# Kernel optimization log

Hardware: AMD Instinct MI355X
Metric: run time of the kernel (lower is better)

Reference implementation:

```python
import jax, jax.numpy as jnp
import numpy as np

N_ORDER = 64
SEQ_LEN = 4096
BATCH = 256


def _hippo_scale_buffers(N: int, L: int):
    """Build bilinear-discretized scaled-Legendre (HiPPO-LegS) transition buffers."""
    q = np.arange(N, dtype=np.float64)
    col, row = np.meshgrid(q, q)  # col[i,j]=j, row[i,j]=i
    r = 2 * q + 1
    M = -(np.where(row >= col, r, 0) - np.diag(q))
    T = np.sqrt(np.diag(2 * q + 1))
    A = T @ M @ np.linalg.inv(T)              # (N,N) continuous-time A
    Bv = np.sqrt(2 * q + 1)                   # diag(T) -> continuous-time B vector
    t = np.arange(1, L + 1, dtype=np.float64)
    A_sc = A[None, :, :] / t[:, None, None]   # (L,N,N)
    B_sc = Bv[None, :] / t[:, None]           # (L,N)
    I = np.eye(N, dtype=np.float64)
    Mm = I[None] - 0.5 * A_sc
    Nn = I[None] + 0.5 * A_sc
    A_d = np.linalg.solve(Mm, Nn)                        # (L,N,N)
    B_d = np.linalg.solve(Mm, B_sc[..., None])[..., 0]   # (L,N)
    return A_d.astype(np.float32), B_d.astype(np.float32)


def setup_inputs() -> dict:
    key = jax.random.key(0)
    inputs = jax.random.normal(key, (SEQ_LEN, BATCH), dtype=jnp.float32)
    A_np, B_np = _hippo_scale_buffers(N_ORDER, SEQ_LEN)
    return {
        "inputs": inputs,
        "A_stacked": jnp.asarray(A_np),   # (L,N,N)
        "B_stacked": jnp.asarray(B_np),   # (L,N)
    }


def reference(inputs, A_stacked, B_stacked):
    """x_t = A_t @ x_{t-1} + B_t * inputs_t, x_{-1} = 0. Returns (L, B, N)."""
    L = inputs.shape[0]
    # u[t, b, :] = inputs[t, b] * B_stacked[t, :]
    u = inputs[..., None] * B_stacked[:L, None, :]  # (L,B,N)

    def step(x, au):
        A_t, u_t = au                                  # (N,N), (B,N)
        x = u_t + jnp.einsum('ij,bj->bi', A_t, x)      # (B,N)
        return x, x

    x0 = jnp.zeros(u.shape[1:], dtype=u.dtype)
    _, xs = jax.lax.scan(step, x0, (A_stacked[:L], u))
    return xs  # (L,B,N)
```

## Files before the change

kernel.cpp:

```cpp
#include <hip/hip_runtime.h>
#include <cstdint>


#define TID ((int)threadIdx.x)

typedef _Float16 half8 __attribute__((ext_vector_type(8)));
typedef _Float16 half4v __attribute__((ext_vector_type(4)));
typedef float f32x4 __attribute__((ext_vector_type(4)));

constexpr int SUBL  = 16;
constexpr int PAD   = 68;

constexpr size_t WS_W = 0;
constexpr size_t WS_Q = 262144;
constexpr size_t WS_P = WS_Q + 1048576;
constexpr size_t WS_Z = WS_P + 262144;
constexpr size_t WS_H = WS_Z + 1048576;
constexpr size_t OLD_WS_FLOATS = WS_H + 1048576;

constexpr int SLOT   = 20480;
constexpr int APITCH = 144;
constexpr int AL_OFF = 9216;
constexpr int BV_OFF = 18432;
constexpr int U_OFF  = 18688;
constexpr size_t AWS_BYTES = (size_t)4096 * SLOT;

__device__ __forceinline__ void stage64x64(const float* __restrict__ g, float* __restrict__ l) {
#pragma unroll
  for (int r = 0; r < 4; ++r) {
    int id = TID + 256 * r;
    int i = id >> 4, j0 = (id & 15) << 2;
    *reinterpret_cast<float4*>(&l[i * PAD + j0]) =
        *reinterpret_cast<const float4*>(&g[i * 64 + j0]);
  }
}

__device__ __forceinline__ void matmul_tile(const float* __restrict__ Ml,
                                            const float* __restrict__ Al,
                                            float* __restrict__ Dl,
                                            int i_lo, int i_hi) {
  float acc[4][4];
#pragma unroll
  for (int a = 0; a < 4; ++a)
#pragma unroll
    for (int b = 0; b < 4; ++b) acc[a][b] = 0.f;
  const int j0 = i_hi << 2;
#pragma unroll
  for (int kq = 0; kq < 16; ++kq) {
    const int k0 = kq << 2;
    float4 mf[4], af[4];
#pragma unroll
    for (int a = 0; a < 4; ++a)
      mf[a] = *reinterpret_cast<const float4*>(&Ml[(i_lo + 16 * a) * PAD + k0]);
#pragma unroll
    for (int kk = 0; kk < 4; ++kk)
      af[kk] = *reinterpret_cast<const float4*>(&Al[(k0 + kk) * PAD + j0]);
#pragma unroll
    for (int a = 0; a < 4; ++a) {
      acc[a][0] += mf[a].x * af[0].x + mf[a].y * af[1].x + mf[a].z * af[2].x + mf[a].w * af[3].x;
      acc[a][1] += mf[a].x * af[0].y + mf[a].y * af[1].y + mf[a].z * af[2].y + mf[a].w * af[3].y;
      acc[a][2] += mf[a].x * af[0].z + mf[a].y * af[1].z + mf[a].z * af[2].z + mf[a].w * af[3].z;
      acc[a][3] += mf[a].x * af[0].w + mf[a].y * af[1].w + mf[a].z * af[2].w + mf[a].w * af[3].w;
    }
  }
#pragma unroll
  for (int a = 0; a < 4; ++a)
    *reinterpret_cast<float4*>(&Dl[(i_lo + 16 * a) * PAD + j0]) =
        make_float4(acc[a][0], acc[a][1], acc[a][2], acc[a][3]);
}

__global__ __launch_bounds__(256) void k0_prep(const float* __restrict__ Ag,
                                               const float* __restrict__ Bg,
                                               const float* __restrict__ inp,
                                               unsigned char* __restrict__ Aws) {
  const int t = blockIdx.x;
  unsigned char* slot = Aws + (size_t)t * SLOT;
  const int i = TID >> 2, jq = TID & 3, j0 = jq << 4;
  const float* arow = Ag + (size_t)t * 4096 + i * 64 + j0;
  half8 hv[2], lv[2];
#pragma unroll
  for (int hf = 0; hf < 2; ++hf) {
#pragma unroll
    for (int r = 0; r < 2; ++r) {
      float4 v = *reinterpret_cast<const float4*>(arow + hf * 8 + r * 4);
      float vv[4] = {v.x, v.y, v.z, v.w};
#pragma unroll
      for (int e = 0; e < 4; ++e) {
        _Float16 h = (_Float16)vv[e];
        hv[hf][r * 4 + e] = h;
        lv[hf][r * 4 + e] = (_Float16)(vv[e] - (float)h);
      }
    }
  }
  *reinterpret_cast<half8*>(slot + i * APITCH + j0 * 2)           = hv[0];
  *reinterpret_cast<half8*>(slot + i * APITCH + j0 * 2 + 16)      = hv[1];
  *reinterpret_cast<half8*>(slot + AL_OFF + i * APITCH + j0 * 2)      = lv[0];
  *reinterpret_cast<half8*>(slot + AL_OFF + i * APITCH + j0 * 2 + 16) = lv[1];
  if (jq == 3) {
    half8 z = {};
    *reinterpret_cast<half8*>(slot + i * APITCH + 128) = z;
    *reinterpret_cast<half8*>(slot + AL_OFF + i * APITCH + 128) = z;
  }
  if (TID < 16)
    *reinterpret_cast<float4*>(slot + BV_OFF + TID * 16) =
        *reinterpret_cast<const float4*>(Bg + (size_t)t * 64 + TID * 4);
  if (TID >= 64 && TID < 128) {
    int q = TID - 64;
    *reinterpret_cast<float4*>(slot + U_OFF + q * 16) =
        *reinterpret_cast<const float4*>(inp + (size_t)t * 256 + q * 4);
  }
}

__global__ __launch_bounds__(256) void k1_suffix(const float* __restrict__ Ag,
                                                 const float* __restrict__ Bg,
                                                 float* __restrict__ W,
                                                 float* __restrict__ Qw) {
  __shared__ float Ms[2][64 * PAD];
  __shared__ float As[64 * PAD];
  __shared__ float Bvs[64];
  const int c = blockIdx.x;
  const int i_lo = TID & 15, i_hi = TID >> 4;
  for (int idx = TID; idx < 64 * PAD; idx += 256) Ms[0][idx] = 0.f;
  __syncthreads();
  if (TID < 64) Ms[0][TID * PAD + TID] = 1.f;
  int cur = 0;
  for (int k = SUBL - 1; k >= 0; --k) {
    const int t = c * SUBL + k;
    stage64x64(Ag + (size_t)t * 4096, As);
    if (TID < 16)
      *reinterpret_cast<float4*>(&Bvs[TID * 4]) =
          *reinterpret_cast<const float4*>(&Bg[t * 64 + TID * 4]);
    __syncthreads();
    if (TID < 64) {
      float wv = 0.f;
#pragma unroll
      for (int kq = 0; kq < 16; ++kq) {
        float4 m = *reinterpret_cast<const float4*>(&Ms[cur][TID * PAD + kq * 4]);
        float4 b = *reinterpret_cast<const float4*>(&Bvs[kq * 4]);
        wv += m.x * b.x + m.y * b.y + m.z * b.z + m.w * b.w;
      }
      W[t * 64 + TID] = wv;
    }
    matmul_tile(Ms[cur], As, Ms[cur ^ 1], i_lo, i_hi);
    __syncthreads();
    cur ^= 1;
  }
#pragma unroll
  for (int r = 0; r < 4; ++r) {
    int id = TID + 256 * r;
    int i = id >> 4, j0 = (id & 15) << 2;
    *reinterpret_cast<float4*>(&Qw[(size_t)c * 4096 + i * 64 + j0]) =
        *reinterpret_cast<const float4*>(&Ms[cur][i * PAD + j0]);
  }
}

__global__ __launch_bounds__(256) void k1b_combine(const float* __restrict__ Qw,
                                                   float* __restrict__ W,
                                                   float* __restrict__ Pw) {
  __shared__ float R[2][64 * PAD];
  __shared__ float Qs[64 * PAD];
  __shared__ float wm[16 * PAD];
  const int s = blockIdx.x;
  const int i_lo = TID & 15, i_hi = TID >> 4;
  int cur = 0;
  for (int m = 3; m >= 0; --m) {
    const int c = 4 * s + m;
    stage64x64(Qw + (size_t)c * 4096, Qs);
    {
      int tt = TID >> 4, i0 = (TID & 15) << 2;
      *reinterpret_cast<float4*>(&wm[tt * PAD + i0]) =
          *reinterpret_cast<const float4*>(&W[(size_t)(c * 16 + tt) * 64 + i0]);
    }
    __syncthreads();
    if (m < 3) {
      float acc[4] = {0.f, 0.f, 0.f, 0.f};
#pragma unroll
      for (int kq = 0; kq < 16; ++kq) {
        const int k0 = kq << 2;
        float4 wf = *reinterpret_cast<const float4*>(&wm[i_hi * PAD + k0]);
#pragma unroll
        for (int a = 0; a < 4; ++a) {
          float4 rf = *reinterpret_cast<const float4*>(&R[cur][(i_lo + 16 * a) * PAD + k0]);
          acc[a] += rf.x * wf.x + rf.y * wf.y + rf.z * wf.z + rf.w * wf.w;
        }
      }
#pragma unroll
      for (int a = 0; a < 4; ++a)
        W[(size_t)(c * 16 + i_hi) * 64 + i_lo + 16 * a] = acc[a];
      matmul_tile(R[cur], Qs, R[cur ^ 1], i_lo, i_hi);
    } else {
#pragma unroll
      for (int r = 0; r < 4; ++r) {
        int id = TID + 256 * r;
        int i = id >> 4, j0 = (id & 15) << 2;
        *reinterpret_cast<float4*>(&R[cur ^ 1][i * PAD + j0]) =
            *reinterpret_cast<const float4*>(&Qs[i * PAD + j0]);
      }
    }
    __syncthreads();
    cur ^= 1;
  }
#pragma unroll
  for (int r = 0; r < 4; ++r) {
    int id = TID + 256 * r;
    int i = id >> 4, j0 = (id & 15) << 2;
    *reinterpret_cast<float4*>(&Pw[(size_t)s * 4096 + i * 64 + j0]) =
        *reinterpret_cast<const float4*>(&R[cur][i * PAD + j0]);
  }
}

__global__ __launch_bounds__(256) void k1c_zgemm(const float* __restrict__ inp,
                                                 const float* __restrict__ W,
                                                 float* __restrict__ Zw) {
  __shared__ float inT[64 * PAD];
  __shared__ float wm[64 * PAD];
  const int s = blockIdx.x >> 2, g = blockIdx.x & 3;
  const int b0 = 64 * g, t0 = s * 64;
  const int i_lo = TID & 15, i_hi = TID >> 4;
#pragma unroll
  for (int r = 0; r < 4; ++r) {
    int id = TID + 256 * r;
    int tl = id >> 4, b4 = (id & 15) << 2;
    float4 v = *reinterpret_cast<const float4*>(&inp[(size_t)(t0 + tl) * 256 + b0 + b4]);
    inT[(b4 + 0) * PAD + tl] = v.x;
    inT[(b4 + 1) * PAD + tl] = v.y;
    inT[(b4 + 2) * PAD + tl] = v.z;
    inT[(b4 + 3) * PAD + tl] = v.w;
  }
#pragma unroll
  for (int r = 0; r < 4; ++r) {
    int id = TID + 256 * r;
    int tl = id >> 4, i0 = (id & 15) << 2;
    *reinterpret_cast<float4*>(&wm[tl * PAD + i0]) =
        *reinterpret_cast<const float4*>(&W[(size_t)(t0 + tl) * 64 + i0]);
  }
  __syncthreads();
  float acc[4][4];
#pragma unroll
  for (int a = 0; a < 4; ++a)
#pragma unroll
    for (int q = 0; q < 4; ++q) acc[a][q] = 0.f;
  const int j0c = i_hi << 2;
#pragma unroll
  for (int kq = 0; kq < 16; ++kq) {
    const int k0 = kq << 2;
    float4 bf[4], wf[4];
#pragma unroll
    for (int a = 0; a < 4; ++a)
      bf[a] = *reinterpret_cast<const float4*>(&inT[(i_lo + 16 * a) * PAD + k0]);
#pragma unroll
    for (int kk = 0; kk < 4; ++kk)
      wf[kk] = *reinterpret_cast<const float4*>(&wm[(k0 + kk) * PAD + j0c]);
#pragma unroll
    for (int a = 0; a < 4; ++a) {
      acc[a][0] += bf[a].x * wf[0].x + bf[a].y * wf[1].x + bf[a].z * wf[2].x + bf[a].w * wf[3].x;
      acc[a][1] += bf[a].x * wf[0].y + bf[a].y * wf[1].y + bf[a].z * wf[2].y + bf[a].w * wf[3].y;
      acc[a][2] += bf[a].x * wf[0].z + bf[a].y * wf[1].z + bf[a].z * wf[2].z + bf[a].w * wf[3].z;
      acc[a][3] += bf[a].x * wf[0].w + bf[a].y * wf[1].w + bf[a].z * wf[2].w + bf[a].w * wf[3].w;
    }
  }
  __syncthreads();
#pragma unroll
  for (int a = 0; a < 4; ++a)
    *reinterpret_cast<float4*>(&wm[(i_lo + 16 * a) * PAD + j0c]) =
        make_float4(acc[a][0], acc[a][1], acc[a][2], acc[a][3]);
  __syncthreads();
#pragma unroll
  for (int r = 0; r < 4; ++r) {
    int id = TID + 256 * r;
    int bl = id >> 4, i0 = (id & 15) << 2;
    *reinterpret_cast<float4*>(&Zw[(size_t)s * 16384 + (b0 + bl) * 64 + i0]) =
        *reinterpret_cast<const float4*>(&wm[bl * PAD + i0]);
  }
}

__global__ __launch_bounds__(256) void k2_carry(const float* __restrict__ Pw,
                                                const float* __restrict__ Zw,
                                                float* __restrict__ Hw) {
  __shared__ float Pt[64 * PAD];
  __shared__ float xb[4 * PAD];
  const int g = blockIdx.x;
  const int bl = TID >> 6, i = TID & 63;
  const int bg = 4 * g + bl;
  for (int idx = TID; idx < 4 * PAD; idx += 256) xb[idx] = 0.f;
#pragma unroll
  for (int r = 0; r < 4; ++r) {
    int id = TID + 256 * r;
    int ir = id >> 4, j0 = (id & 15) << 2;
    float4 v = *reinterpret_cast<const float4*>(&Pw[ir * 64 + j0]);
    Pt[(j0 + 0) * PAD + ir] = v.x;
    Pt[(j0 + 1) * PAD + ir] = v.y;
    Pt[(j0 + 2) * PAD + ir] = v.z;
    Pt[(j0 + 3) * PAD + ir] = v.w;
  }
  __syncthreads();
  float h = 0.f;
  for (int s = 0; s < 64; ++s) {
    Hw[(size_t)s * 16384 + bg * 64 + i] = h;
    float acc = Zw[(size_t)s * 16384 + bg * 64 + i];
#pragma unroll
    for (int jq = 0; jq < 16; ++jq) {
      const int j0 = jq << 2;
      float4 xf = *reinterpret_cast<const float4*>(&xb[bl * PAD + j0]);
      acc += Pt[(j0 + 0) * PAD + i] * xf.x + Pt[(j0 + 1) * PAD + i] * xf.y +
             Pt[(j0 + 2) * PAD + i] * xf.z + Pt[(j0 + 3) * PAD + i] * xf.w;
    }
    h = acc;
    __syncthreads();
    xb[bl * PAD + i] = h;
    if (s < 63) {
#pragma unroll
      for (int r = 0; r < 4; ++r) {
        int id = TID + 256 * r;
        int ir = id >> 4, j0 = (id & 15) << 2;
        float4 v = *reinterpret_cast<const float4*>(&Pw[(size_t)(s + 1) * 4096 + ir * 64 + j0]);
        Pt[(j0 + 0) * PAD + ir] = v.x;
        Pt[(j0 + 1) * PAD + ir] = v.y;
        Pt[(j0 + 2) * PAD + ir] = v.z;
        Pt[(j0 + 3) * PAD + ir] = v.w;
      }
    }
    __syncthreads();
  }
}

__global__ __launch_bounds__(256) void k3_final(const float* __restrict__ Ag,
                                                const float* __restrict__ Bg,
                                                const float* __restrict__ inp,
                                                const float* __restrict__ Hw,
                                                float* __restrict__ out) {
  __shared__ float As[64 * PAD];
  __shared__ float xs[64 * PAD];
  __shared__ float Bvs[64];
  __shared__ float ins[64];
  const int s = blockIdx.x >> 2, g = blockIdx.x & 3;
  const int b0 = 64 * g;
  const int i_lo = TID & 15, i_hi = TID >> 4;
#pragma unroll
  for (int r = 0; r < 4; ++r) {
    int id = TID + 256 * r;
    int bl = id >> 4, i0 = (id & 15) << 2;
    *reinterpret_cast<float4*>(&xs[bl * PAD + i0]) =
        *reinterpret_cast<const float4*>(&Hw[(size_t)s * 16384 + (b0 + bl) * 64 + i0]);
  }
  for (int k = 0; k < 64; ++k) {
    const int t = s * 64 + k;
    stage64x64(Ag + (size_t)t * 4096, As);
    if (TID < 16)
      *reinterpret_cast<float4*>(&Bvs[TID * 4]) =
          *reinterpret_cast<const float4*>(&Bg[t * 64 + TID * 4]);
    if (TID >= 64 && TID < 80) {
      int q = TID - 64;
      *reinterpret_cast<float4*>(&ins[q * 4]) =
          *reinterpret_cast<const float4*>(&inp[(size_t)t * 256 + b0 + q * 4]);
    }
    __syncthreads();
    float acc[4][4];
#pragma unroll
    for (int a = 0; a < 4; ++a)
#pragma unroll
      for (int r = 0; r < 4; ++r) acc[a][r] = 0.f;
#pragma unroll
    for (int jq = 0; jq < 16; ++jq) {
      const int j0 = jq << 2;
      float4 af[4], xf[4];
#pragma unroll
      for (int a = 0; a < 4; ++a)
        af[a] = *reinterpret_cast<const float4*>(&As[(i_lo + 16 * a) * PAD + j0]);
#pragma unroll
      for (int r = 0; r < 4; ++r)
        xf[r] = *reinterpret_cast<const float4*>(&xs[(i_hi + 16 * r) * PAD + j0]);
#pragma unroll
      for (int a = 0; a < 4; ++a)
#pragma unroll
        for (int r = 0; r < 4; ++r)
          acc[a][r] += af[a].x * xf[r].x + af[a].y * xf[r].y + af[a].z * xf[r].z + af[a].w * xf[r].w;
    }
    float bv[4], ui[4];
#pragma unroll
    for (int a = 0; a < 4; ++a) bv[a] = Bvs[i_lo + 16 * a];
#pragma unroll
    for (int r = 0; r < 4; ++r) ui[r] = ins[i_hi + 16 * r];
#pragma unroll
    for (int a = 0; a < 4; ++a)
#pragma unroll
      for (int r = 0; r < 4; ++r) acc[a][r] += bv[a] * ui[r];
    __syncthreads();
#pragma unroll
    for (int r = 0; r < 4; ++r)
#pragma unroll
      for (int a = 0; a < 4; ++a)
        xs[(i_hi + 16 * r) * PAD + i_lo + 16 * a] = acc[a][r];
    __syncthreads();
#pragma unroll
    for (int r = 0; r < 4; ++r) {
      int id = TID + 256 * r;
      int bl = id >> 4, i0 = (id & 15) << 2;
      *reinterpret_cast<float4*>(&out[((size_t)t * 256 + b0 + bl) * 64 + i0]) =
          *reinterpret_cast<const float4*>(&xs[bl * PAD + i0]);
    }
  }
}

__device__ __forceinline__ void gload_lds16(const void* g, void* l) {
  __builtin_amdgcn_global_load_lds(
      (const __attribute__((address_space(1))) unsigned int*)g,
      (__attribute__((address_space(3))) unsigned int*)l, 16, 0, 0);
}

constexpr int LDS_XH = 2 * SLOT;
constexpr int LDS_XL = LDS_XH + 9216;
constexpr int LDS_SZ = LDS_XL + 9216;

__global__ __launch_bounds__(256) void k3_mfma(const unsigned char* __restrict__ Aws,
                                               const float* __restrict__ Hw,
                                               float* __restrict__ out) {
  __shared__ __align__(16) unsigned char sm[LDS_SZ];
  const int blk = blockIdx.x;
  const int s = (blk & 7) | ((blk >> 5) << 3);
  const int g = (blk >> 3) & 3;
  const int b0 = g << 6;
  const int lane = TID & 63, wave = TID >> 6;
  const int lm = lane & 15, quad = lane >> 4;
  const int wm = wave >> 1, wn = wave & 1;

#pragma unroll
  for (int r = 0; r < 4; ++r) {
    int id = TID + (r << 8);
    int bl = id >> 4, j0 = (id & 15) << 2;
    float4 v = *reinterpret_cast<const float4*>(
        &Hw[(size_t)s * 16384 + (size_t)(b0 + bl) * 64 + j0]);
    float vv[4] = {v.x, v.y, v.z, v.w};
    half4v hh, ll;
#pragma unroll
    for (int e = 0; e < 4; ++e) {
      _Float16 h = (_Float16)vv[e];
      hh[e] = h;
      ll[e] = (_Float16)(vv[e] - (float)h);
    }
    *reinterpret_cast<half4v*>(sm + LDS_XH + bl * APITCH + (j0 << 1)) = hh;
    *reinterpret_cast<half4v*>(sm + LDS_XL + bl * APITCH + (j0 << 1)) = ll;
  }

  const size_t t0 = (size_t)s * 64;
  {
    const unsigned char* gsl = Aws + t0 * SLOT;
#pragma unroll
    for (int r = 0; r < 5; ++r) {
      int off = ((r << 2) + wave) << 10;
      gload_lds16(gsl + off + lane * 16, sm + off);
    }
  }

  int aoff[2][2], xoffh[2][2], xoffl[2][2], woff[2][2];
#pragma unroll
  for (int mt = 0; mt < 2; ++mt)
#pragma unroll
    for (int kt = 0; kt < 2; ++kt)
      aoff[mt][kt] = ((wm << 5) + (mt << 4) + lm) * APITCH + (((kt << 5) + (quad << 3)) << 1);
#pragma unroll
  for (int nt = 0; nt < 2; ++nt)
#pragma unroll
    for (int kt = 0; kt < 2; ++kt) {
      int o = ((wn << 5) + (nt << 4) + lm) * APITCH + (((kt << 5) + (quad << 3)) << 1);
      xoffh[nt][kt] = LDS_XH + o;
      xoffl[nt][kt] = LDS_XL + o;
    }
#pragma unroll
  for (int nt = 0; nt < 2; ++nt)
#pragma unroll
    for (int mt = 0; mt < 2; ++mt)
      woff[nt][mt] = ((wn << 5) + (nt << 4) + lm) * APITCH +
                     (((wm << 5) + (mt << 4) + (quad << 2)) << 1);

  __syncthreads();

  int cur = 0;
  for (int k = 0; k < 64; ++k) {
    const unsigned char* ab = sm + cur * SLOT;
    if (k < 63) {
      const unsigned char* gsl = Aws + (t0 + k + 1) * SLOT;
      unsigned char* lb = sm + (cur ^ 1) * SLOT;
#pragma unroll
      for (int r = 0; r < 5; ++r) {
        int off = ((r << 2) + wave) << 10;
        gload_lds16(gsl + off + lane * 16, lb + off);
      }
    }
    half8 fa[2][2], fal[2][2], fxh[2][2], fxl[2][2];
#pragma unroll
    for (int mt = 0; mt < 2; ++mt)
#pragma unroll
      for (int kt = 0; kt < 2; ++kt) {
        fa[mt][kt]  = *reinterpret_cast<const half8*>(ab + aoff[mt][kt]);
        fal[mt][kt] = *reinterpret_cast<const half8*>(ab + AL_OFF + aoff[mt][kt]);
      }
#pragma unroll
    for (int nt = 0; nt < 2; ++nt)
#pragma unroll
      for (int kt = 0; kt < 2; ++kt) {
        fxh[nt][kt] = *reinterpret_cast<const half8*>(sm + xoffh[nt][kt]);
        fxl[nt][kt] = *reinterpret_cast<const half8*>(sm + xoffl[nt][kt]);
      }
    float4 bv[2];
#pragma unroll
    for (int mt = 0; mt < 2; ++mt)
      bv[mt] = *reinterpret_cast<const float4*>(
          ab + BV_OFF + (((wm << 5) + (mt << 4) + (quad << 2)) << 2));
    float uu[2];
#pragma unroll
    for (int nt = 0; nt < 2; ++nt)
      uu[nt] = *reinterpret_cast<const float*>(
          ab + U_OFF + ((b0 + (wn << 5) + (nt << 4) + lm) << 2));

    f32x4 acc[2][2] = {};
#pragma unroll
    for (int mt = 0; mt < 2; ++mt)
#pragma unroll
      for (int nt = 0; nt < 2; ++nt)
#pragma unroll
        for (int kt = 0; kt < 2; ++kt) {
          acc[mt][nt] = __builtin_amdgcn_mfma_f32_16x16x32_f16(fa[mt][kt],  fxh[nt][kt], acc[mt][nt], 0, 0, 0);
          acc[mt][nt] = __builtin_amdgcn_mfma_f32_16x16x32_f16(fal[mt][kt], fxh[nt][kt], acc[mt][nt], 0, 0, 0);
          acc[mt][nt] = __builtin_amdgcn_mfma_f32_16x16x32_f16(fa[mt][kt],  fxl[nt][kt], acc[mt][nt], 0, 0, 0);
        }
#pragma unroll
    for (int mt = 0; mt < 2; ++mt) {
      const float* bp = reinterpret_cast<const float*>(&bv[mt]);
#pragma unroll
      for (int nt = 0; nt < 2; ++nt)
#pragma unroll
        for (int e = 0; e < 4; ++e) acc[mt][nt][e] += bp[e] * uu[nt];
    }
    __syncthreads();
#pragma unroll
    for (int mt = 0; mt < 2; ++mt)
#pragma unroll
      for (int nt = 0; nt < 2; ++nt) {
        half4v hh, ll;
#pragma unroll
        for (int e = 0; e < 4; ++e) {
          float x = acc[mt][nt][e];
          _Float16 h = (_Float16)x;
          hh[e] = h;
          ll[e] = (_Float16)(x - (float)h);
        }
        *reinterpret_cast<half4v*>(sm + LDS_XH + woff[nt][mt]) = hh;
        *reinterpret_cast<half4v*>(sm + LDS_XL + woff[nt][mt]) = ll;
        const int bglob = b0 + (wn << 5) + (nt << 4) + lm;
        const int irow = (wm << 5) + (mt << 4) + (quad << 2);
        *reinterpret_cast<float4*>(&out[(((t0 + k) << 8) + bglob) * 64 + irow]) =
            make_float4(acc[mt][nt][0], acc[mt][nt][1], acc[mt][nt][2], acc[mt][nt][3]);
      }
    __syncthreads();
    cur ^= 1;
  }
}

extern "C" void kernel_launch(void* const* d_in, const int* in_sizes, int n_in,
                              void* d_out, int out_size, void* d_ws, size_t ws_size,
                              hipStream_t stream) {
  const float* inputs = (const float*)d_in[0];
  const float* Ag     = (const float*)d_in[1];
  const float* Bg     = (const float*)d_in[2];
  float* out = (float*)d_out;

  const bool use_mfma = ws_size >= AWS_BYTES + OLD_WS_FLOATS * 4;
  unsigned char* Aws = (unsigned char*)d_ws;
  float* ws = (float*)((char*)d_ws + (use_mfma ? AWS_BYTES : 0));
  float* W  = ws + WS_W;
  float* Qw = ws + WS_Q;
  float* Pw = ws + WS_P;
  float* Zw = ws + WS_Z;
  float* Hw = ws + WS_H;

  if (use_mfma) k0_prep<<<4096, 256, 0, stream>>>(Ag, Bg, inputs, Aws);
  k1_suffix<<<256, 256, 0, stream>>>(Ag, Bg, W, Qw);
  k1b_combine<<<64, 256, 0, stream>>>(Qw, W, Pw);
  k1c_zgemm<<<256, 256, 0, stream>>>(inputs, W, Zw);
  k2_carry<<<64, 256, 0, stream>>>(Pw, Zw, Hw);
  if (use_mfma)
    k3_mfma<<<256, 256, 0, stream>>>(Aws, Hw, out);
  else
    k3_final<<<256, 256, 0, stream>>>(Ag, Bg, inputs, Hw, out);
}
```

Before: 644.8 us.

## Fuse A-prep into suffix kernel, prefetch carry loads, split final MFMA grid

The separate A_t split/conversion kernel is folded into the suffix-product kernel, so each A_t is read from global memory once and written out as hi/lo fp16 in the same pass that forms the chunk products. The suffix kernel also double-buffers A_t and B_t in shared memory, and the carry kernel prefetches the next P and Z values into registers before the current step. The final MFMA kernel halves the batch tile per block to 32 columns and launches 512 blocks with two blocks per CU, trading per-block reuse for more parallelism. This removes one launch and one full read of A, at the cost of more shared memory and register use in the fused kernel.

```diff
diff --git a/kernel.cpp b/kernel.cpp
--- a/kernel.cpp
+++ b/kernel.cpp
@@ -69,45 +69,109 @@
         make_float4(acc[a][0], acc[a][1], acc[a][2], acc[a][3]);
 }
 
-__global__ __launch_bounds__(256) void k0_prep(const float* __restrict__ Ag,
-                                               const float* __restrict__ Bg,
-                                               const float* __restrict__ inp,
-                                               unsigned char* __restrict__ Aws) {
-  const int t = blockIdx.x;
-  unsigned char* slot = Aws + (size_t)t * SLOT;
-  const int i = TID >> 2, jq = TID & 3, j0 = jq << 4;
-  const float* arow = Ag + (size_t)t * 4096 + i * 64 + j0;
-  half8 hv[2], lv[2];
-#pragma unroll
-  for (int hf = 0; hf < 2; ++hf) {
-#pragma unroll
-    for (int r = 0; r < 2; ++r) {
-      float4 v = *reinterpret_cast<const float4*>(arow + hf * 8 + r * 4);
-      float vv[4] = {v.x, v.y, v.z, v.w};
+__global__ __launch_bounds__(256) void k1_fused(const float* __restrict__ Ag,
+                                                const float* __restrict__ Bg,
+                                                const float* __restrict__ inp,
+                                                unsigned char* __restrict__ Aws,
+                                                float* __restrict__ W,
+                                                float* __restrict__ Qw) {
+  __shared__ float Ms[2][64 * PAD];
+  __shared__ float As[2][64 * PAD];
+  __shared__ float Bvs[2][64];
+  const int c = blockIdx.x;
+  const int i_lo = TID & 15, i_hi = TID >> 4;
+  const int r_i0 = TID >> 4;
+  const int r_j0 = (TID & 15) << 2;
+
+  for (int idx = TID; idx < 64 * PAD; idx += 256) Ms[0][idx] = 0.f;
+
+  float4 pc[4];
+  float4 bvc = make_float4(0.f, 0.f, 0.f, 0.f);
+  {
+    const float* g = Ag + (size_t)(c * SUBL + SUBL - 1) * 4096;
+#pragma unroll
+    for (int r = 0; r < 4; ++r)
+      pc[r] = *reinterpret_cast<const float4*>(&g[(r_i0 + 16 * r) * 64 + r_j0]);
+    if (TID < 16)
+      bvc = *reinterpret_cast<const float4*>(&Bg[(size_t)(c * SUBL + SUBL - 1) * 64 + TID * 4]);
+  }
+  __syncthreads();
+  if (TID < 64) Ms[0][TID * PAD + TID] = 1.f;
+#pragma unroll
+  for (int r = 0; r < 4; ++r)
+    *reinterpret_cast<float4*>(&As[0][(r_i0 + 16 * r) * PAD + r_j0]) = pc[r];
+  if (TID < 16) *reinterpret_cast<float4*>(&Bvs[0][TID * 4]) = bvc;
+  __syncthreads();
+
+  int cur = 0, ab = 0;
+  for (int k = SUBL - 1; k >= 0; --k) {
+    const int t = c * SUBL + k;
+    unsigned char* slot = Aws + (size_t)t * SLOT;
+    float4 pn[4];
+    float4 bvn = make_float4(0.f, 0.f, 0.f, 0.f);
+    if (k > 0) {
+      const float* g = Ag + (size_t)(t - 1) * 4096;
+#pragma unroll
+      for (int r = 0; r < 4; ++r)
+        pn[r] = *reinterpret_cast<const float4*>(&g[(r_i0 + 16 * r) * 64 + r_j0]);
+      if (TID < 16)
+        bvn = *reinterpret_cast<const float4*>(&Bg[(size_t)(t - 1) * 64 + TID * 4]);
+    }
+    if (TID >= 64 && TID < 128) {
+      int q = TID - 64;
+      *reinterpret_cast<float4*>(slot + U_OFF + q * 16) =
+          *reinterpret_cast<const float4*>(inp + (size_t)t * 256 + q * 4);
+    }
+    if (TID < 16) *reinterpret_cast<float4*>(slot + BV_OFF + TID * 16) = bvc;
+    if (TID < 64) {
+      float wv = 0.f;
+#pragma unroll
+      for (int kq = 0; kq < 16; ++kq) {
+        float4 m = *reinterpret_cast<const float4*>(&Ms[cur][TID * PAD + kq * 4]);
+        float4 b = *reinterpret_cast<const float4*>(&Bvs[ab][kq * 4]);
+        wv += m.x * b.x + m.y * b.y + m.z * b.z + m.w * b.w;
+      }
+      W[t * 64 + TID] = wv;
+    }
+#pragma unroll
+    for (int r = 0; r < 4; ++r) {
+      float vv[4] = {pc[r].x, pc[r].y, pc[r].z, pc[r].w};
+      half4v hh, ll;
 #pragma unroll
       for (int e = 0; e < 4; ++e) {
         _Float16 h = (_Float16)vv[e];
-        hv[hf][r * 4 + e] = h;
-        lv[hf][r * 4 + e] = (_Float16)(vv[e] - (float)h);
-      }
-    }
-  }
-  *reinterpret_cast<half8*>(slot + i * APITCH + j0 * 2)           = hv[0];
-  *reinterpret_cast<half8*>(slot + i * APITCH + j0 * 2 + 16)      = hv[1];
-  *reinterpret_cast<half8*>(slot + AL_OFF + i * APITCH + j0 * 2)      = lv[0];
-  *reinterpret_cast<half8*>(slot + AL_OFF + i * APITCH + j0 * 2 + 16) = lv[1];
-  if (jq == 3) {
-    half8 z = {};
-    *reinterpret_cast<half8*>(slot + i * APITCH + 128) = z;
-    *reinterpret_cast<half8*>(slot + AL_OFF + i * APITCH + 128) = z;
-  }
-  if (TID < 16)
-    *reinterpret_cast<float4*>(slot + BV_OFF + TID * 16) =
-        *reinterpret_cast<const float4*>(Bg + (size_t)t * 64 + TID * 4);
-  if (TID >= 64 && TID < 128) {
-    int q = TID - 64;
-    *reinterpret_cast<float4*>(slot + U_OFF + q * 16) =
-        *reinterpret_cast<const float4*>(inp + (size_t)t * 256 + q * 4);
+        hh[e] = h;
+        ll[e] = (_Float16)(vv[e] - (float)h);
+      }
+      const int row = r_i0 + 16 * r;
+      *reinterpret_cast<half4v*>(slot + row * APITCH + r_j0 * 2) = hh;
+      *reinterpret_cast<half4v*>(slot + AL_OFF + row * APITCH + r_j0 * 2) = ll;
+    }
+    if (TID < 64) {
+      half8 z = {};
+      *reinterpret_cast<half8*>(slot + TID * APITCH + 128) = z;
+      *reinterpret_cast<half8*>(slot + AL_OFF + TID * APITCH + 128) = z;
+    }
+    matmul_tile(Ms[cur], As[ab], Ms[cur ^ 1], i_lo, i_hi);
+    if (k > 0) {
+#pragma unroll
+      for (int r = 0; r < 4; ++r)
+        *reinterpret_cast<float4*>(&As[ab ^ 1][(r_i0 + 16 * r) * PAD + r_j0]) = pn[r];
+      if (TID < 16) *reinterpret_cast<float4*>(&Bvs[ab ^ 1][TID * 4]) = bvn;
+#pragma unroll
+      for (int r = 0; r < 4; ++r) pc[r] = pn[r];
+      bvc = bvn;
+    }
+    __syncthreads();
+    cur ^= 1;
+    ab ^= 1;
+  }
+#pragma unroll
+  for (int r = 0; r < 4; ++r) {
+    int id = TID + 256 * r;
+    int i = id >> 4, j0 = (id & 15) << 2;
+    *reinterpret_cast<float4*>(&Qw[(size_t)c * 4096 + i * 64 + j0]) =
+        *reinterpret_cast<const float4*>(&Ms[cur][i * PAD + j0]);
   }
 }
 
@@ -282,28 +346,41 @@
   const int g = blockIdx.x;
   const int bl = TID >> 6, i = TID & 63;
   const int bg = 4 * g + bl;
+  const int ir = TID >> 4, j0 = (TID & 15) << 2;
   for (int idx = TID; idx < 4 * PAD; idx += 256) xb[idx] = 0.f;
-#pragma unroll
-  for (int r = 0; r < 4; ++r) {
-    int id = TID + 256 * r;
-    int ir = id >> 4, j0 = (id & 15) << 2;
-    float4 v = *reinterpret_cast<const float4*>(&Pw[ir * 64 + j0]);
-    Pt[(j0 + 0) * PAD + ir] = v.x;
-    Pt[(j0 + 1) * PAD + ir] = v.y;
-    Pt[(j0 + 2) * PAD + ir] = v.z;
-    Pt[(j0 + 3) * PAD + ir] = v.w;
+  float4 p0[4];
+#pragma unroll
+  for (int r = 0; r < 4; ++r)
+    p0[r] = *reinterpret_cast<const float4*>(&Pw[(ir + 16 * r) * 64 + j0]);
+  float zc = Zw[(size_t)bg * 64 + i];
+#pragma unroll
+  for (int r = 0; r < 4; ++r) {
+    int row = ir + 16 * r;
+    Pt[(j0 + 0) * PAD + row] = p0[r].x;
+    Pt[(j0 + 1) * PAD + row] = p0[r].y;
+    Pt[(j0 + 2) * PAD + row] = p0[r].z;
+    Pt[(j0 + 3) * PAD + row] = p0[r].w;
   }
   __syncthreads();
   float h = 0.f;
   for (int s = 0; s < 64; ++s) {
+    float4 pn[4];
+    float zn = 0.f;
+    if (s < 63) {
+#pragma unroll
+      for (int r = 0; r < 4; ++r)
+        pn[r] = *reinterpret_cast<const float4*>(
+            &Pw[(size_t)(s + 1) * 4096 + (ir + 16 * r) * 64 + j0]);
+      zn = Zw[(size_t)(s + 1) * 16384 + bg * 64 + i];
+    }
     Hw[(size_t)s * 16384 + bg * 64 + i] = h;
-    float acc = Zw[(size_t)s * 16384 + bg * 64 + i];
+    float acc = zc;
 #pragma unroll
     for (int jq = 0; jq < 16; ++jq) {
-      const int j0 = jq << 2;
-      float4 xf = *reinterpret_cast<const float4*>(&xb[bl * PAD + j0]);
-      acc += Pt[(j0 + 0) * PAD + i] * xf.x + Pt[(j0 + 1) * PAD + i] * xf.y +
-             Pt[(j0 + 2) * PAD + i] * xf.z + Pt[(j0 + 3) * PAD + i] * xf.w;
+      const int jj = jq << 2;
+      float4 xf = *reinterpret_cast<const float4*>(&xb[bl * PAD + jj]);
+      acc += Pt[(jj + 0) * PAD + i] * xf.x + Pt[(jj + 1) * PAD + i] * xf.y +
+             Pt[(jj + 2) * PAD + i] * xf.z + Pt[(jj + 3) * PAD + i] * xf.w;
     }
     h = acc;
     __syncthreads();
@@ -311,14 +388,13 @@
     if (s < 63) {
 #pragma unroll
       for (int r = 0; r < 4; ++r) {
-        int id = TID + 256 * r;
-        int ir = id >> 4, j0 = (id & 15) << 2;
-        float4 v = *reinterpret_cast<const float4*>(&Pw[(size_t)(s + 1) * 4096 + ir * 64 + j0]);
-        Pt[(j0 + 0) * PAD + ir] = v.x;
-        Pt[(j0 + 1) * PAD + ir] = v.y;
-        Pt[(j0 + 2) * PAD + ir] = v.z;
-        Pt[(j0 + 3) * PAD + ir] = v.w;
-      }
+        int row = ir + 16 * r;
+        Pt[(j0 + 0) * PAD + row] = pn[r].x;
+        Pt[(j0 + 1) * PAD + row] = pn[r].y;
+        Pt[(j0 + 2) * PAD + row] = pn[r].z;
+        Pt[(j0 + 3) * PAD + row] = pn[r].w;
+      }
+      zc = zn;
     }
     __syncthreads();
   }
@@ -408,24 +484,25 @@
       (__attribute__((address_space(3))) unsigned int*)l, 16, 0, 0);
 }
 
+constexpr int XROWS  = 32;
 constexpr int LDS_XH = 2 * SLOT;
-constexpr int LDS_XL = LDS_XH + 9216;
-constexpr int LDS_SZ = LDS_XL + 9216;
-
-__global__ __launch_bounds__(256) void k3_mfma(const unsigned char* __restrict__ Aws,
-                                               const float* __restrict__ Hw,
-                                               float* __restrict__ out) {
+constexpr int LDS_XL = LDS_XH + XROWS * APITCH;
+constexpr int LDS_SZ = LDS_XL + XROWS * APITCH;
+
+__global__ __launch_bounds__(256, 2) void k3_mfma(const unsigned char* __restrict__ Aws,
+                                                  const float* __restrict__ Hw,
+                                                  float* __restrict__ out) {
   __shared__ __align__(16) unsigned char sm[LDS_SZ];
   const int blk = blockIdx.x;
-  const int s = (blk & 7) | ((blk >> 5) << 3);
-  const int g = (blk >> 3) & 3;
-  const int b0 = g << 6;
+  const int s = (blk & 7) | ((blk >> 6) << 3);
+  const int g = (blk >> 3) & 7;
+  const int b0 = g << 5;
   const int lane = TID & 63, wave = TID >> 6;
   const int lm = lane & 15, quad = lane >> 4;
   const int wm = wave >> 1, wn = wave & 1;
 
 #pragma unroll
-  for (int r = 0; r < 4; ++r) {
+  for (int r = 0; r < 2; ++r) {
     int id = TID + (r << 8);
     int bl = id >> 4, j0 = (id & 15) << 2;
     float4 v = *reinterpret_cast<const float4*>(
@@ -452,26 +529,21 @@
     }
   }
 
-  int aoff[2][2], xoffh[2][2], xoffl[2][2], woff[2][2];
+  int aoff[2][2], xoffh[2], xoffl[2], woff[2];
 #pragma unroll
   for (int mt = 0; mt < 2; ++mt)
 #pragma unroll
     for (int kt = 0; kt < 2; ++kt)
       aoff[mt][kt] = ((wm << 5) + (mt << 4) + lm) * APITCH + (((kt << 5) + (quad << 3)) << 1);
 #pragma unroll
-  for (int nt = 0; nt < 2; ++nt)
-#pragma unroll
-    for (int kt = 0; kt < 2; ++kt) {
-      int o = ((wn << 5) + (nt << 4) + lm) * APITCH + (((kt << 5) + (quad << 3)) << 1);
-      xoffh[nt][kt] = LDS_XH + o;
-      xoffl[nt][kt] = LDS_XL + o;
-    }
-#pragma unroll
-  for (int nt = 0; nt < 2; ++nt)
-#pragma unroll
-    for (int mt = 0; mt < 2; ++mt)
-      woff[nt][mt] = ((wn << 5) + (nt << 4) + lm) * APITCH +
-                     (((wm << 5) + (mt << 4) + (quad << 2)) << 1);
+  for (int kt = 0; kt < 2; ++kt) {
+    int o = ((wn << 4) + lm) * APITCH + (((kt << 5) + (quad << 3)) << 1);
+    xoffh[kt] = LDS_XH + o;
+    xoffl[kt] = LDS_XL + o;
+  }
+#pragma unroll
+  for (int mt = 0; mt < 2; ++mt)
+    woff[mt] = ((wn << 4) + lm) * APITCH + (((wm << 5) + (mt << 4) + (quad << 2)) << 1);
 
   __syncthreads();
 
@@ -487,7 +559,7 @@
         gload_lds16(gsl + off + lane * 16, lb + off);
       }
     }
-    half8 fa[2][2], fal[2][2], fxh[2][2], fxl[2][2];
+    half8 fa[2][2], fal[2][2], fxh[2], fxl[2];
 #pragma unroll
     for (int mt = 0; mt < 2; ++mt)
 #pragma unroll
@@ -496,62 +568,51 @@
         fal[mt][kt] = *reinterpret_cast<const half8*>(ab + AL_OFF + aoff[mt][kt]);
       }
 #pragma unroll
-    for (int nt = 0; nt < 2; ++nt)
-#pragma unroll
-      for (int kt = 0; kt < 2; ++kt) {
-        fxh[nt][kt] = *reinterpret_cast<const half8*>(sm + xoffh[nt][kt]);
-        fxl[nt][kt] = *reinterpret_cast<const half8*>(sm + xoffl[nt][kt]);
-      }
+    for (int kt = 0; kt < 2; ++kt) {
+      fxh[kt] = *reinterpret_cast<const half8*>(sm + xoffh[kt]);
+      fxl[kt] = *reinterpret_cast<const half8*>(sm + xoffl[kt]);
+    }
     float4 bv[2];
 #pragma unroll
     for (int mt = 0; mt < 2; ++mt)
       bv[mt] = *reinterpret_cast<const float4*>(
           ab + BV_OFF + (((wm << 5) + (mt << 4) + (quad << 2)) << 2));
-    float uu[2];
-#pragma unroll
-    for (int nt = 0; nt < 2; ++nt)
-      uu[nt] = *reinterpret_cast<const float*>(
-          ab + U_OFF + ((b0 + (wn << 5) + (nt << 4) + lm) << 2));
-
-    f32x4 acc[2][2] = {};
+    float uu = *reinterpret_cast<const float*>(
+        ab + U_OFF + ((b0 + (wn << 4) + lm) << 2));
+
+    f32x4 acc[2] = {};
 #pragma unroll
     for (int mt = 0; mt < 2; ++mt)
 #pragma unroll
-      for (int nt = 0; nt < 2; ++nt)
-#pragma unroll
-        for (int kt = 0; kt < 2; ++kt) {
-          acc[mt][nt] = __builtin_amdgcn_mfma_f32_16x16x32_f16(fa[mt][kt],  fxh[nt][kt], acc[mt][nt], 0, 0, 0);
-          acc[mt][nt] = __builtin_amdgcn_mfma_f32_16x16x32_f16(fal[mt][kt], fxh[nt][kt], acc[mt][nt], 0, 0, 0);
-          acc[mt][nt] = __builtin_amdgcn_mfma_f32_16x16x32_f16(fa[mt][kt],  fxl[nt][kt], acc[mt][nt], 0, 0, 0);
-        }
+      for (int kt = 0; kt < 2; ++kt) {
+        acc[mt] = __builtin_amdgcn_mfma_f32_16x16x32_f16(fa[mt][kt],  fxh[kt], acc[mt], 0, 0, 0);
+        acc[mt] = __builtin_amdgcn_mfma_f32_16x16x32_f16(fal[mt][kt], fxh[kt], acc[mt], 0, 0, 0);
+        acc[mt] = __builtin_amdgcn_mfma_f32_16x16x32_f16(fa[mt][kt],  fxl[kt], acc[mt], 0, 0, 0);
+      }
 #pragma unroll
     for (int mt = 0; mt < 2; ++mt) {
       const float* bp = reinterpret_cast<const float*>(&bv[mt]);
 #pragma unroll
-      for (int nt = 0; nt < 2; ++nt)
-#pragma unroll
-        for (int e = 0; e < 4; ++e) acc[mt][nt][e] += bp[e] * uu[nt];
-    }
-    __syncthreads();
-#pragma unroll
-    for (int mt = 0; mt < 2; ++mt)
-#pragma unroll
-      for (int nt = 0; nt < 2; ++nt) {
-        half4v hh, ll;
-#pragma unroll
-        for (int e = 0; e < 4; ++e) {
-          float x = acc[mt][nt][e];
-          _Float16 h = (_Float16)x;
-          hh[e] = h;
-          ll[e] = (_Float16)(x - (float)h);
-        }
-        *reinterpret_cast<half4v*>(sm + LDS_XH + woff[nt][mt]) = hh;
-        *reinterpret_cast<half4v*>(sm + LDS_XL + woff[nt][mt]) = ll;
-        const int bglob = b0 + (wn << 5) + (nt << 4) + lm;
-        const int irow = (wm << 5) + (mt << 4) + (quad << 2);
-        *reinterpret_cast<float4*>(&out[(((t0 + k) << 8) + bglob) * 64 + irow]) =
-            make_float4(acc[mt][nt][0], acc[mt][nt][1], acc[mt][nt][2], acc[mt][nt][3]);
-      }
+      for (int e = 0; e < 4; ++e) acc[mt][e] += bp[e] * uu;
+    }
+    __syncthreads();
+#pragma unroll
+    for (int mt = 0; mt < 2; ++mt) {
+      half4v hh, ll;
+#pragma unroll
+      for (int e = 0; e < 4; ++e) {
+        float x = acc[mt][e];
+        _Float16 h = (_Float16)x;
+        hh[e] = h;
+        ll[e] = (_Float16)(x - (float)h);
+      }
+      *reinterpret_cast<half4v*>(sm + LDS_XH + woff[mt]) = hh;
+      *reinterpret_cast<half4v*>(sm + LDS_XL + woff[mt]) = ll;
+      const int bglob = b0 + (wn << 4) + lm;
+      const int irow = (wm << 5) + (mt << 4) + (quad << 2);
+      *reinterpret_cast<float4*>(&out[(((t0 + k) << 8) + bglob) * 64 + irow]) =
+          make_float4(acc[mt][0], acc[mt][1], acc[mt][2], acc[mt][3]);
+    }
     __syncthreads();
     cur ^= 1;
   }
@@ -574,13 +635,15 @@
   float* Zw = ws + WS_Z;
   float* Hw = ws + WS_H;
 
-  if (use_mfma) k0_prep<<<4096, 256, 0, stream>>>(Ag, Bg, inputs, Aws);
-  k1_suffix<<<256, 256, 0, stream>>>(Ag, Bg, W, Qw);
+  if (use_mfma)
+    k1_fused<<<256, 256, 0, stream>>>(Ag, Bg, inputs, Aws, W, Qw);
+  else
+    k1_suffix<<<256, 256, 0, stream>>>(Ag, Bg, W, Qw);
   k1b_combine<<<64, 256, 0, stream>>>(Qw, W, Pw);
   k1c_zgemm<<<256, 256, 0, stream>>>(inputs, W, Zw);
   k2_carry<<<64, 256, 0, stream>>>(Pw, Zw, Hw);
   if (use_mfma)
-    k3_mfma<<<256, 256, 0, stream>>>(Aws, Hw, out);
+    k3_mfma<<<512, 256, 0, stream>>>(Aws, Hw, out);
   else
     k3_final<<<256, 256, 0, stream>>>(Ag, Bg, inputs, Hw, out);
 }
```

Result: faster. 581.7 us (-9.8%).
